# Kernel optimization log

Measured on AMD Instinct MI355X. Metric: run time of the kernel, lower is better.

The kernel has to match this reference:

```python
import jax, jax.numpy as jnp
import numpy as np

SCALES = (3, 9, 17, 33)  # must be odd so padding=s//2 preserves spatial size


def _box_conv(img, s):
    # img: [B,1,H,W]; conv with an all-ones s x s kernel, 'same' padding for odd s
    k = jnp.ones((1, 1, s, s), img.dtype)
    p = s // 2
    return jax.lax.conv_general_dilated(
        img, k, window_strides=(1, 1), padding=[(p, p), (p, p)],
        dimension_numbers=("NCHW", "OIHW", "NCHW"))


def setup_inputs() -> dict:
    key = jax.random.key(0)
    B, C, H, W = 8, 3, 1024, 1024
    x = jax.random.normal(key, (B, C, H, W), dtype=jnp.float32)
    # mimicking sparse path-traced samples
    keep = jax.random.uniform(jax.random.fold_in(key, 1), (B, 1, H, W)) >= 0.3
    x = jnp.where(keep, x, 0.0)
    return {"x": x}


def reference(x):
    # F.conv2d(x, ones(1,3,1,1)/3) == per-pixel mean over the 3 channels
    lum = jnp.mean(x, axis=1, keepdims=True)          # [B,1,H,W]
    nonzero = (lum != 0).astype(lum.dtype)            # [B,1,H,W]
    feats = []
    for s in SCALES:
        count = _box_conv(nonzero, s)                 # number of nonzero pixels in window
        pool = _box_conv(lum, s) / jnp.maximum(count, 1.0)  # mean over nonzero pixels
        feats.append(count / float(s * s))            # percentage of nonzero pixels
        feats.append(pool)
    return jnp.concatenate(feats, axis=1)             # [B, 2*len(SCALES), H, W]
```

## Files before the change

### kernel.cpp

```cpp
#include <hip/hip_runtime.h>


constexpr int W_    = 1024;
constexpr int H_    = 1024;
constexpr int PAD   = 17;
constexpr int PROWS = H_ + 2 * PAD;
constexpr int RS2   = 64;

template<int CTRL, int RM>
__device__ __forceinline__ int dppadd_i(int v) {
    int sh = __builtin_amdgcn_update_dpp(0, v, CTRL, RM, 0xF, true);
    return v + sh;
}

__device__ __forceinline__ int wave_iscan_i(int v) {
    v = dppadd_i<0x111, 0xF>(v);
    v = dppadd_i<0x112, 0xF>(v);
    v = dppadd_i<0x114, 0xF>(v);
    v = dppadd_i<0x118, 0xF>(v);
    v = dppadd_i<0x142, 0xA>(v);
    v = dppadd_i<0x143, 0xC>(v);
    return v;
}

__global__ __launch_bounds__(256)
void prefix_kernel(const float* __restrict__ x, unsigned int* __restrict__ P,
                   int B) {
    const int lane = threadIdx.x & 63;
    const int wv   = threadIdx.x >> 6;
    const int rp   = blockIdx.x * 4 + wv;
    const int b    = blockIdx.z;
    if (rp >= PROWS) return;

    unsigned int* prow = P + ((size_t)b * PROWS + rp) * W_;
    const int r = rp - PAD;

    if (r < 0 || r >= H_) {
        #pragma unroll
        for (int c = 0; c < 16; ++c) prow[c * 64 + lane] = 0u;
        return;
    }

    const size_t HW = (size_t)H_ * W_;
    const float* px = x + (size_t)b * 3 * HW + (size_t)r * W_;

    float L[16];
    #pragma unroll
    for (int c = 0; c < 16; ++c) {
        const int col = c * 64 + lane;
        L[c] = (px[col] + px[col + HW] + px[col + 2 * HW]) * (1.0f / 3.0f);
    }

    int carry = 0;
    #pragma unroll
    for (int c = 0; c < 16; ++c) {
        const float lum = L[c];
        int val = ((int)rintf(lum * 1024.f) << 16) | ((lum != 0.f) ? 1 : 0);
        int s = wave_iscan_i(val) + carry;
        prow[c * 64 + lane] = (unsigned int)s;
        carry = __shfl(s, 63);
    }
}

__global__ __launch_bounds__(256)
void emit_kernel(const unsigned int* __restrict__ P, float* __restrict__ out,
                 int B) {
    constexpr int   PP[4]   = {1, 4, 8, 16};
    constexpr float INVA[4] = {1.f/9.f, 1.f/81.f, 1.f/289.f, 1.f/1089.f};
    constexpr float INVQ    = 1.f / 1024.f;

    const int t  = threadIdx.x;
    const int x  = blockIdx.x * 256 + t;
    const int y0 = blockIdx.y * RS2;
    const int b  = blockIdx.z;

    const unsigned int* Pb = P + (size_t)b * PROWS * W_;
    const size_t HW = (size_t)H_ * W_;
    float* outb = out + (size_t)b * 8 * HW + x;

    int x1c[4], x2c[4]; bool ok[4];
    #pragma unroll
    for (int i = 0; i < 4; ++i) {
        const int p  = PP[i];
        const int x1 = x - p - 1;
        ok[i]  = (x1 >= 0);
        x1c[i] = max(x1, 0);
        x2c[i] = min(x + p, W_ - 1);
    }

    auto rd = [&](int y, int i) -> unsigned int {
        const unsigned int* rw = Pb + (size_t)(y + PAD) * W_;
        unsigned int hi = rw[x2c[i]];
        unsigned int lo = ok[i] ? rw[x1c[i]] : 0u;
        return hi - lo;
    };

    int vl[4], vn[4];
    #pragma unroll
    for (int i = 0; i < 4; ++i) {
        const int p = PP[i];
        int sl = 0, sn = 0;
        for (int yy = y0 - 1 - p; yy <= y0 - 1 + p; ++yy) {
            unsigned int df = rd(yy, i);
            sl += (int)df >> 16;
            sn += (int)(df & 0xFFFFu);
        }
        vl[i] = sl; vn[i] = sn;
    }

    #pragma unroll 2
    for (int y = y0; y < y0 + RS2; ++y) {
        #pragma unroll
        for (int i = 0; i < 4; ++i) {
            const int p = PP[i];
            unsigned int e = rd(y + p, i);
            unsigned int l = rd(y - 1 - p, i);
            vl[i] += ((int)e >> 16) - ((int)l >> 16);
            vn[i] += (int)(e & 0xFFFFu) - (int)(l & 0xFFFFu);
        }
        float* o = outb + (size_t)y * W_;
        #pragma unroll
        for (int i = 0; i < 4; ++i) {
            float cnt = (float)vn[i];
            o[(size_t)(2 * i) * HW]     = cnt * INVA[i];
            o[(size_t)(2 * i + 1) * HW] =
                (float)vl[i] * INVQ * __builtin_amdgcn_rcpf(fmaxf(cnt, 1.f));
        }
    }
}

extern "C" void kernel_launch(void* const* d_in, const int* in_sizes, int n_in,
                              void* d_out, int out_size, void* d_ws, size_t ws_size,
                              hipStream_t stream) {
    const float* x   = (const float*)d_in[0];
    float*       out = (float*)d_out;

    const int B = in_sizes[0] / (3 * H_ * W_);
    unsigned int* P = (unsigned int*)d_ws;

    dim3 g1((PROWS + 3) / 4, 1, B);
    prefix_kernel<<<g1, dim3(256), 0, stream>>>(x, P, B);

    dim3 g2(W_ / 256, H_ / RS2, B);
    emit_kernel<<<g2, dim3(256), 0, stream>>>(P, out, B);
}
```

Baseline: 128.9 us.

## Pad prefix rows and vectorize prefix/emit kernels with 4-wide loads and stores

Prefix rows are padded with zeros on the left and replicated totals on the right, so emit no longer needs bounds clamping. Both kernels now process 4 adjacent columns per thread using float4/uint4 loads and stores. Each emit block covers a full 1024-wide row strip of 8 rows, and strips are ordered in a swizzled row sequence. The shorter strips mean more redundant vertical warm-up sums per block, and the unaligned 16-byte loads at offsets like p and -p-1 may split across cache lines.

```diff
diff --git a/kernel.cpp b/kernel.cpp
--- a/kernel.cpp
+++ b/kernel.cpp
@@ -5,7 +5,9 @@
 constexpr int H_    = 1024;
 constexpr int PAD   = 17;
 constexpr int PROWS = H_ + 2 * PAD;
-constexpr int RS2   = 64;
+constexpr int LPAD  = 20;
+constexpr int RW    = 1064;
+constexpr int RS2   = 8;
 
 template<int CTRL, int RM>
 __device__ __forceinline__ int dppadd_i(int v) {
@@ -23,89 +25,102 @@
     return v;
 }
 
+__device__ __forceinline__ void ld4(const unsigned int* p, unsigned int r[4]) {
+    __builtin_memcpy(r, p, 16);
+}
+
 __global__ __launch_bounds__(256)
-void prefix_kernel(const float* __restrict__ x, unsigned int* __restrict__ P,
-                   int B) {
+void prefix_kernel(const float* __restrict__ x, unsigned int* __restrict__ P) {
     const int lane = threadIdx.x & 63;
     const int wv   = threadIdx.x >> 6;
     const int rp   = blockIdx.x * 4 + wv;
-    const int b    = blockIdx.z;
+    const int b    = blockIdx.y;
     if (rp >= PROWS) return;
 
-    unsigned int* prow = P + ((size_t)b * PROWS + rp) * W_;
+    unsigned int* prow = P + ((size_t)b * PROWS + rp) * RW;
     const int r = rp - PAD;
 
     if (r < 0 || r >= H_) {
-        #pragma unroll
-        for (int c = 0; c < 16; ++c) prow[c * 64 + lane] = 0u;
+        uint4 z = make_uint4(0u, 0u, 0u, 0u);
+        for (int i = lane; i < RW / 4; i += 64)
+            ((uint4*)prow)[i] = z;
         return;
     }
 
     const size_t HW = (size_t)H_ * W_;
     const float* px = x + (size_t)b * 3 * HW + (size_t)r * W_;
 
-    float L[16];
+    int carry = 0;
     #pragma unroll
-    for (int c = 0; c < 16; ++c) {
-        const int col = c * 64 + lane;
-        L[c] = (px[col] + px[col + HW] + px[col + 2 * HW]) * (1.0f / 3.0f);
+    for (int c = 0; c < 4; ++c) {
+        const int col = c * 256 + 4 * lane;
+        float4 r0 = *(const float4*)(px + col);
+        float4 r1 = *(const float4*)(px + col + HW);
+        float4 r2 = *(const float4*)(px + col + 2 * HW);
+        float l0 = (r0.x + r1.x + r2.x) * (1.0f / 3.0f);
+        float l1 = (r0.y + r1.y + r2.y) * (1.0f / 3.0f);
+        float l2 = (r0.z + r1.z + r2.z) * (1.0f / 3.0f);
+        float l3 = (r0.w + r1.w + r2.w) * (1.0f / 3.0f);
+        int v0 = ((int)rintf(l0 * 1024.f) << 16) | ((l0 != 0.f) ? 1 : 0);
+        int v1 = ((int)rintf(l1 * 1024.f) << 16) | ((l1 != 0.f) ? 1 : 0);
+        int v2 = ((int)rintf(l2 * 1024.f) << 16) | ((l2 != 0.f) ? 1 : 0);
+        int v3 = ((int)rintf(l3 * 1024.f) << 16) | ((l3 != 0.f) ? 1 : 0);
+        int s0 = v0, s1 = s0 + v1, s2 = s1 + v2, s3 = s2 + v3;
+        int incl = wave_iscan_i(s3);
+        int excl = incl - s3 + carry;
+        uint4 o = make_uint4((unsigned)(excl + s0), (unsigned)(excl + s1),
+                             (unsigned)(excl + s2), (unsigned)(excl + s3));
+        *(uint4*)(prow + LPAD + col) = o;
+        carry += __shfl(incl, 63);
     }
 
-    int carry = 0;
-    #pragma unroll
-    for (int c = 0; c < 16; ++c) {
-        const float lum = L[c];
-        int val = ((int)rintf(lum * 1024.f) << 16) | ((lum != 0.f) ? 1 : 0);
-        int s = wave_iscan_i(val) + carry;
-        prow[c * 64 + lane] = (unsigned int)s;
-        carry = __shfl(s, 63);
+    const unsigned int total = (unsigned int)carry;
+    if (lane < 5) {
+        *(uint4*)(prow + 4 * lane) = make_uint4(0u, 0u, 0u, 0u);
+    } else if (lane < 10) {
+        const int i = lane - 5;
+        *(uint4*)(prow + LPAD + W_ + 4 * i) =
+            make_uint4(total, total, total, total);
     }
 }
 
-__global__ __launch_bounds__(256)
-void emit_kernel(const unsigned int* __restrict__ P, float* __restrict__ out,
-                 int B) {
+__global__ __launch_bounds__(256, 4)
+void emit_kernel(const unsigned int* __restrict__ P, float* __restrict__ out) {
     constexpr int   PP[4]   = {1, 4, 8, 16};
     constexpr float INVA[4] = {1.f/9.f, 1.f/81.f, 1.f/289.f, 1.f/1089.f};
     constexpr float INVQ    = 1.f / 1024.f;
 
     const int t  = threadIdx.x;
-    const int x  = blockIdx.x * 256 + t;
-    const int y0 = blockIdx.y * RS2;
-    const int b  = blockIdx.z;
+    const int x0 = 4 * t;
 
-    const unsigned int* Pb = P + (size_t)b * PROWS * W_;
+    const int bx = blockIdx.x;
+    const int yt = (bx & 7) * 16 + (bx >> 3);
+    const int y0 = yt * RS2;
+    const int b  = blockIdx.y;
+
+    const unsigned int* Pb = P + (size_t)b * PROWS * RW;
     const size_t HW = (size_t)H_ * W_;
-    float* outb = out + (size_t)b * 8 * HW + x;
+    float* outb = out + (size_t)b * 8 * HW;
 
-    int x1c[4], x2c[4]; bool ok[4];
-    #pragma unroll
-    for (int i = 0; i < 4; ++i) {
-        const int p  = PP[i];
-        const int x1 = x - p - 1;
-        ok[i]  = (x1 >= 0);
-        x1c[i] = max(x1, 0);
-        x2c[i] = min(x + p, W_ - 1);
-    }
+    auto rowp = [&](int y) { return Pb + (size_t)(y + PAD) * RW + LPAD + x0; };
 
-    auto rd = [&](int y, int i) -> unsigned int {
-        const unsigned int* rw = Pb + (size_t)(y + PAD) * W_;
-        unsigned int hi = rw[x2c[i]];
-        unsigned int lo = ok[i] ? rw[x1c[i]] : 0u;
-        return hi - lo;
-    };
-
-    int vl[4], vn[4];
+    int vl[4][4], vn[4][4];
     #pragma unroll
     for (int i = 0; i < 4; ++i) {
         const int p = PP[i];
-        int sl = 0, sn = 0;
+        #pragma unroll
+        for (int j = 0; j < 4; ++j) { vl[i][j] = 0; vn[i][j] = 0; }
         for (int yy = y0 - 1 - p; yy <= y0 - 1 + p; ++yy) {
-            unsigned int df = rd(yy, i);
-            sl += (int)df >> 16;
-            sn += (int)(df & 0xFFFFu);
+            const unsigned int* rw = rowp(yy);
+            unsigned int hi[4], lo[4];
+            ld4(rw + p, hi); ld4(rw - p - 1, lo);
+            #pragma unroll
+            for (int j = 0; j < 4; ++j) {
+                unsigned int df = hi[j] - lo[j];
+                vl[i][j] += (int)df >> 16;
+                vn[i][j] += (int)(df & 0xFFFFu);
+            }
         }
-        vl[i] = sl; vn[i] = sn;
     }
 
     #pragma unroll 2
@@ -113,18 +128,33 @@
         #pragma unroll
         for (int i = 0; i < 4; ++i) {
             const int p = PP[i];
-            unsigned int e = rd(y + p, i);
-            unsigned int l = rd(y - 1 - p, i);
-            vl[i] += ((int)e >> 16) - ((int)l >> 16);
-            vn[i] += (int)(e & 0xFFFFu) - (int)(l & 0xFFFFu);
+            const unsigned int* re = rowp(y + p);
+            const unsigned int* rl = rowp(y - 1 - p);
+            unsigned int eh[4], el[4], lh[4], ll[4];
+            ld4(re + p, eh); ld4(re - p - 1, el);
+            ld4(rl + p, lh); ld4(rl - p - 1, ll);
+            #pragma unroll
+            for (int j = 0; j < 4; ++j) {
+                unsigned int de = eh[j] - el[j];
+                unsigned int dg = lh[j] - ll[j];
+                vl[i][j] += ((int)de >> 16) - ((int)dg >> 16);
+                vn[i][j] += (int)(de & 0xFFFFu) - (int)(dg & 0xFFFFu);
+            }
         }
-        float* o = outb + (size_t)y * W_;
+        float* orow = outb + (size_t)y * W_ + x0;
         #pragma unroll
         for (int i = 0; i < 4; ++i) {
-            float cnt = (float)vn[i];
-            o[(size_t)(2 * i) * HW]     = cnt * INVA[i];
-            o[(size_t)(2 * i + 1) * HW] =
-                (float)vl[i] * INVQ * __builtin_amdgcn_rcpf(fmaxf(cnt, 1.f));
+            float c0 = (float)vn[i][0], c1 = (float)vn[i][1];
+            float c2 = (float)vn[i][2], c3 = (float)vn[i][3];
+            float4 cnt4 = make_float4(c0 * INVA[i], c1 * INVA[i],
+                                      c2 * INVA[i], c3 * INVA[i]);
+            float4 pool4 = make_float4(
+                (float)vl[i][0] * INVQ * __builtin_amdgcn_rcpf(fmaxf(c0, 1.f)),
+                (float)vl[i][1] * INVQ * __builtin_amdgcn_rcpf(fmaxf(c1, 1.f)),
+                (float)vl[i][2] * INVQ * __builtin_amdgcn_rcpf(fmaxf(c2, 1.f)),
+                (float)vl[i][3] * INVQ * __builtin_amdgcn_rcpf(fmaxf(c3, 1.f)));
+            *(float4*)(orow + (size_t)(2 * i) * HW)     = cnt4;
+            *(float4*)(orow + (size_t)(2 * i + 1) * HW) = pool4;
         }
     }
 }
@@ -138,9 +168,9 @@
     const int B = in_sizes[0] / (3 * H_ * W_);
     unsigned int* P = (unsigned int*)d_ws;
 
-    dim3 g1((PROWS + 3) / 4, 1, B);
-    prefix_kernel<<<g1, dim3(256), 0, stream>>>(x, P, B);
+    dim3 g1((PROWS + 3) / 4, B);
+    prefix_kernel<<<g1, dim3(256), 0, stream>>>(x, P);
 
-    dim3 g2(W_ / 256, H_ / RS2, B);
-    emit_kernel<<<g2, dim3(256), 0, stream>>>(P, out, B);
+    dim3 g2(H_ / RS2 / 8 * 8, B);
+    emit_kernel<<<g2, dim3(256), 0, stream>>>(P, out);
 }
```

Result: no change. 129.1 us (+0.1%).
